# Kernel optimization log

Measured on AMD Instinct MI355X. Metric: run time of the kernel, lower is better.

Reference implementation:

```python
import jax, jax.numpy as jnp
import numpy as np

VOCAB = 16000   # code_size
EMBED = 16
HID = 256
B, T = 64, 128


def _glorot(key, shape, fan):
    return jax.random.normal(key, shape, dtype=jnp.float32) / np.sqrt(fan)


def setup_inputs() -> dict:
    key = jax.random.key(0)
    ks = jax.random.split(key, 20)
    inp = {
        "tokens": jax.random.randint(ks[0], (B, T), 0, VOCAB),
        "h0": jax.random.normal(ks[1], (B, HID), dtype=jnp.float32),
        "c0": jax.random.normal(ks[2], (B, HID), dtype=jnp.float32),
        "emb": jax.random.normal(ks[3], (VOCAB, EMBED), dtype=jnp.float32),
        # LSTMCell params, PyTorch layout: W_ih [4H, in], W_hh [4H, H], biases [4H]
        "Wih1": _glorot(ks[4], (4 * HID, EMBED), EMBED),
        "Whh1": _glorot(ks[5], (4 * HID, HID), HID),
        "bih1": jnp.zeros((4 * HID,), jnp.float32),
        "bhh1": jnp.zeros((4 * HID,), jnp.float32),
        "Wih2": _glorot(ks[6], (4 * HID, HID), HID),
        "Whh2": _glorot(ks[7], (4 * HID, HID), HID),
        "bih2": jnp.zeros((4 * HID,), jnp.float32),
        "bhh2": jnp.zeros((4 * HID,), jnp.float32),
        "Wih3": _glorot(ks[8], (4 * HID, HID), HID),
        "Whh3": _glorot(ks[9], (4 * HID, HID), HID),
        "bih3": jnp.zeros((4 * HID,), jnp.float32),
        "bhh3": jnp.zeros((4 * HID,), jnp.float32),
        # head: Linear(HID,HID) -> ReLU -> Linear(HID,VOCAB)
        "W1": _glorot(ks[10], (HID, HID), HID),
        "b1": jnp.zeros((HID,), jnp.float32),
        "W2": _glorot(ks[11], (VOCAB, HID), HID),
        "b2": jnp.zeros((VOCAB,), jnp.float32),
    }
    return inp


def _lstm_cell(x, h, c, Wih, Whh, bih, bhh):
    # PyTorch LSTMCell gate order: i, f, g, o
    gates = x @ Wih.T + bih + h @ Whh.T + bhh          # [B, 4H]
    i, f, g, o = jnp.split(gates, 4, axis=-1)
    i, f, o = jax.nn.sigmoid(i), jax.nn.sigmoid(f), jax.nn.sigmoid(o)
    g = jnp.tanh(g)
    c_new = f * c + i * g
    h_new = o * jnp.tanh(c_new)
    return h_new, c_new


def reference(tokens, h0, c0, emb,
              Wih1, Whh1, bih1, bhh1,
              Wih2, Whh2, bih2, bhh2,
              Wih3, Whh3, bih3, bhh3,
              W1, b1, W2, b2):
    Bn, Tn = tokens.shape
    x = emb[tokens]                       # [B, T, E]
    xs = jnp.swapaxes(x, 0, 1)            # [T, B, E] for scan over time

    def step(carry, x_t):
        h1, c1, h2, c2, h3, c3 = carry
        h1, c1 = _lstm_cell(x_t, h1, c1, Wih1, Whh1, bih1, bhh1)
        h2, c2 = _lstm_cell(h1, h2, c2, Wih2, Whh2, bih2, bhh2)
        h3, c3 = _lstm_cell(h2, h3, c3, Wih3, Whh3, bih3, bhh3)
        score = jax.nn.relu(h3 @ W1.T + b1) @ W2.T + b2   # [B, V]
        return (h1, c1, h2, c2, h3, c3), score

    init = (h0, c0, h0, c0, h0, c0)       # hidden1 = hidden2 = hidden3 = hidden
    _, scores = jax.lax.scan(step, init, xs)              # [T, B, V]
    scores = jnp.swapaxes(scores, 0, 1).reshape(Bn * Tn, -1)
    labels = tokens.reshape(-1)
    return scores, labels
```

## Files before the change

kernel.cpp:

```cpp
#include <hip/hip_runtime.h>
#include <hip/hip_bf16.h>
#include <stdint.h>

#define T_SEQ 128
#define BATCH 64
#define HIDN  256
#define EMB   16
#define VOCAB 16000
#define HSTR  40

typedef __attribute__((ext_vector_type(8))) short short8v;
typedef __attribute__((ext_vector_type(4))) float f32x4;
typedef __attribute__((ext_vector_type(4))) unsigned short us4v;
typedef unsigned short ushort_t;
typedef unsigned long long u64_t;

#define OFF_WC1    0
#define OFF_WC2    131072
#define OFF_WC3    393216
#define OFF_BS2    655360
#define OFF_BS3    656384
#define OFF_FLAGS  657408
#define OFF_W1T    658432
#define OFF_H3     723968
#define OFF_S1     2821120
#define OFF_W2BF   3869696

#define OUT_XG     0
#define OUT_RINGS  8388608

#define RING_STRIDE 2113536
#define SLOT 16384

__device__ __forceinline__ ushort_t f2bf(float x) {
    __hip_bfloat16 h = __float2bfloat16(x);
    return *reinterpret_cast<ushort_t*>(&h);
}

__device__ __forceinline__ float dpp_x1(float x) {
    return __builtin_bit_cast(float, __builtin_amdgcn_mov_dpp(
        __builtin_bit_cast(int, x), 0xB1, 0xF, 0xF, true));
}
__device__ __forceinline__ float dpp_x2(float x) {
    return __builtin_bit_cast(float, __builtin_amdgcn_mov_dpp(
        __builtin_bit_cast(int, x), 0x4E, 0xF, 0xF, true));
}
__device__ __forceinline__ f32x4 dpp4_x1(f32x4 v) {
    f32x4 r; r[0]=dpp_x1(v[0]); r[1]=dpp_x1(v[1]); r[2]=dpp_x1(v[2]); r[3]=dpp_x1(v[3]); return r;
}
__device__ __forceinline__ f32x4 dpp4_x2(f32x4 v) {
    f32x4 r; r[0]=dpp_x2(v[0]); r[1]=dpp_x2(v[1]); r[2]=dpp_x2(v[2]); r[3]=dpp_x2(v[3]); return r;
}

__device__ __forceinline__ void spin_ge(const int* p, int target) {
    while (__hip_atomic_load(p, __ATOMIC_RELAXED, __HIP_MEMORY_SCOPE_AGENT) < target) {}
}

__device__ __forceinline__ f32x4 bypass_ld128(const void* p) {
    f32x4 v;
    asm volatile("global_load_dwordx4 %0, %1, off sc0 sc1" : "=v"(v) : "v"((uint64_t)p));
    return v;
}
__device__ __forceinline__ void bypass_st128(void* p, f32x4 v) {
    asm volatile("global_store_dwordx4 %0, %1, off sc0 sc1" :: "v"((uint64_t)p), "v"(v) : "memory");
}
__device__ __forceinline__ void vm_drain() {
    asm volatile("s_waitcnt vmcnt(0)" ::: "memory");
    __builtin_amdgcn_sched_barrier(0);
}
__device__ __forceinline__ void lgkm_drain() {
    asm volatile("s_waitcnt lgkmcnt(0)" ::: "memory");
    __builtin_amdgcn_sched_barrier(0);
}

__global__ void k_reset_flags(float* wsf) {
    ((int*)(wsf + OFF_FLAGS))[threadIdx.x] = 0;
}

__global__ void k_reorder_w(const float* __restrict__ Whh1,
                            const float* __restrict__ Wih2, const float* __restrict__ Whh2,
                            const float* __restrict__ Wih3, const float* __restrict__ Whh3,
                            float* __restrict__ wsf) {
    int bid = blockIdx.x;
    int layer = bid >> 10, c = bid & 1023;
    int wgi = c >> 7, rr = c & 127, jl = rr >> 2, gg = rr & 3;
    int row = gg * 256 + wgi * 32 + jl;
    int tid = threadIdx.x;
    if (layer == 0) {
        ushort_t* dst = (ushort_t*)(wsf + OFF_WC1) + (size_t)c * 256;
        dst[tid] = f2bf(Whh1[row * 256 + tid]);
    } else {
        const float* Wi = (layer == 1) ? Wih2 : Wih3;
        const float* Wh = (layer == 1) ? Whh2 : Whh3;
        ushort_t* dst = (ushort_t*)(wsf + ((layer == 1) ? OFF_WC2 : OFF_WC3)) + (size_t)c * 512;
        for (int k = tid; k < 512; k += 256)
            dst[k] = f2bf(k < 256 ? Wi[row * 256 + k] : Wh[row * 256 + k - 256]);
    }
}

__global__ void k_bias23(const float* __restrict__ bi2, const float* __restrict__ bh2,
                         const float* __restrict__ bi3, const float* __restrict__ bh3,
                         float* __restrict__ wsf) {
    int idx = blockIdx.x * 256 + threadIdx.x;
    int layer = idx >> 10, c = idx & 1023;
    int wgi = c >> 7, rr = c & 127, jl = rr >> 2, gg = rr & 3;
    int row = gg * 256 + wgi * 32 + jl;
    wsf[((layer == 0) ? OFF_BS2 : OFF_BS3) + c] =
        (layer == 0) ? (bi2[row] + bh2[row]) : (bi3[row] + bh3[row]);
}

__global__ void k_xg(const int* __restrict__ tokens, const float* __restrict__ emb,
                     const float* __restrict__ Wih1, const float* __restrict__ bih1,
                     const float* __restrict__ bhh1, float* __restrict__ xg) {
    int t = blockIdx.x, cg = blockIdx.y;
    int tid = threadIdx.x;
    __shared__ float xs[64][16];
    for (int idx = tid; idx < 1024; idx += 256) {
        int b = idx >> 4, e = idx & 15;
        xs[b][e] = emb[(size_t)tokens[b * T_SEQ + t] * 16 + e];
    }
    __syncthreads();
    int c = cg * 64 + (tid & 63);
    int b0 = (tid >> 6) * 16;
    int wgi = c >> 7, rr = c & 127, jl = rr >> 2, gg = rr & 3;
    int row = gg * 256 + wgi * 32 + jl;
    float wv[16];
    #pragma unroll
    for (int e = 0; e < 16; ++e) wv[e] = Wih1[row * 16 + e];
    float bias = bih1[row] + bhh1[row];
    float* dst = xg + ((size_t)t * 1024 + c) * 64 + b0;
    for (int b = 0; b < 16; ++b) {
        float s = bias;
        #pragma unroll
        for (int e = 0; e < 16; ++e) s += xs[b0 + b][e] * wv[e];
        dst[b] = s;
    }
}

__global__ void k_init_rings(const float* __restrict__ h0, ushort_t* __restrict__ rbase) {
    int idx = blockIdx.x * 256 + threadIdx.x;
    ushort_t v = f2bf(h0[idx]);
    rbase[idx] = v;
    rbase[RING_STRIDE + idx] = v;
    rbase[2 * RING_STRIDE + idx] = v;
}

__global__ void k_transpose_w1(const float* __restrict__ src, float* __restrict__ dst) {
    int idx = blockIdx.x * 256 + threadIdx.x;
    int n = idx & 255, k = idx >> 8;
    dst[idx] = src[n * 256 + k];
}

__global__ void k_conv_w2(const float* __restrict__ src, ushort_t* __restrict__ dst, int n) {
    int idx = blockIdx.x * 256 + threadIdx.x;
    if (idx < n) dst[idx] = f2bf(src[idx]);
}

template<int LAYER, int NKS>
__device__ __forceinline__ void lstm_body(
    int wg, int tid, const float* __restrict__ c0,
    float* __restrict__ wsf, float* __restrict__ outf,
    ushort_t* hA, ushort_t* hB, ushort_t* hS) {
    const int w = tid >> 6, lane = tid & 63, lr = lane & 15, lg = lane >> 4;
    const int g = lr & 3;
    const int K = NKS * 32;
    const ushort_t* WC = (const ushort_t*)(wsf + (LAYER == 0 ? OFF_WC1 : LAYER == 1 ? OFF_WC2 : OFF_WC3));
    int* fl = (int*)(wsf + OFF_FLAGS);
    ushort_t* H3b = (ushort_t*)(wsf + OFF_H3);
    const float* xg = outf + OUT_XG;
    ushort_t* rbase = (ushort_t*)(outf + OUT_RINGS);
    ushort_t* ringIn = rbase + (size_t)(LAYER == 0 ? 0 : LAYER - 1) * RING_STRIDE;
    ushort_t* ringOwn = rbase + (size_t)LAYER * RING_STRIDE;

    const int ccol = wg * 128 + 2 * w * 16 + lr;
    short8v wr0[NKS], wr1[NKS];
    #pragma unroll
    for (int ks = 0; ks < NKS; ++ks) {
        wr0[ks] = *(const short8v*)(WC + (size_t)ccol * K + ks * 32 + lg * 8);
        wr1[ks] = *(const short8v*)(WC + (size_t)(ccol + 16) * K + ks * 32 + lg * 8);
    }
    float bs0 = 0.f, bs1 = 0.f;
    if (LAYER > 0) {
        const float* BS = wsf + (LAYER == 1 ? OFF_BS2 : OFF_BS3);
        bs0 = BS[ccol]; bs1 = BS[ccol + 16];
    }
    const int jj0 = w * 8 + (lr >> 2);
    const int j0 = wg * 32 + jj0;
    f32x4 cst[4][2];
    #pragma unroll
    for (int i = 0; i < 4; ++i)
        #pragma unroll
        for (int r = 0; r < 4; ++r) {
            cst[i][0][r] = c0[(i * 16 + lg * 4 + r) * 256 + j0];
            cst[i][1][r] = c0[(i * 16 + lg * 4 + r) * 256 + j0 + 4];
        }

    const float sOwn = (g == 2) ? 2.f : -1.f;
    const float aOwn = (g == 2) ? -2.f : 1.f;
    const float bOwn = (g == 2) ? 1.f : 0.f;

    for (int t = 0; t < T_SEQ; ++t) {
        f32x4 xpre[8];
        if (LAYER == 0) {
            const float* xt = xg + ((size_t)t * 1024 + wg * 128) * 64;
            #pragma unroll
            for (int i = 0; i < 4; ++i) {
                xpre[i]     = *(const f32x4*)(xt + (size_t)(2 * w * 16 + lr) * 64 + i * 16 + lg * 4);
                xpre[i + 4] = *(const f32x4*)(xt + (size_t)((2 * w + 1) * 16 + lr) * 64 + i * 16 + lg * 4);
            }
        }
        if (LAYER == 0) {
            if (tid < 8) spin_ge(&fl[tid], t);
        } else {
            if (tid < 16) {
                int idx = tid & 7;
                const int* p = (tid < 8) ? &fl[(LAYER - 1) * 8 + idx] : &fl[LAYER * 8 + idx];
                spin_ge(p, (tid < 8) ? t + 1 : t);
            }
        }
        __syncthreads();
        {
            const char* sA = (const char*)(LAYER == 0 ? (ringOwn + (size_t)t * SLOT)
                                                      : (ringIn + (size_t)(t + 1) * SLOT));
            f32x4 ta[8], tb[8];
            #pragma unroll
            for (int it = 0; it < 8; ++it)
                ta[it] = bypass_ld128(sA + it * 4096 + tid * 16);
            if (LAYER > 0) {
                const char* sB = (const char*)(ringOwn + (size_t)t * SLOT);
                #pragma unroll
                for (int it = 0; it < 8; ++it)
                    tb[it] = bypass_ld128(sB + it * 4096 + tid * 16);
            }
            vm_drain();
            #pragma unroll
            for (int it = 0; it < 8; ++it) {
                int e16 = it * 256 + tid;
                int row = e16 >> 5, c16 = e16 & 31;
                int off = row * 512 + ((c16 ^ (row & 15)) << 4);
                *(f32x4*)((char*)hA + off) = ta[it];
                if (LAYER > 0) *(f32x4*)((char*)hB + off) = tb[it];
            }
        }
        __syncthreads();
        f32x4 acc[4][2];
        if (LAYER == 0) {
            #pragma unroll
            for (int i = 0; i < 4; ++i) { acc[i][0] = xpre[i]; acc[i][1] = xpre[i + 4]; }
        } else {
            #pragma unroll
            for (int i = 0; i < 4; ++i) {
                acc[i][0] = (f32x4){bs0, bs0, bs0, bs0};
                acc[i][1] = (f32x4){bs1, bs1, bs1, bs1};
            }
        }
        #pragma unroll
        for (int i = 0; i < 4; ++i) {
            #pragma unroll
            for (int ks = 0; ks < NKS; ++ks) {
                const ushort_t* hsrc = (ks < 8) ? hA : hB;
                const int krem = ks & 7;
                short8v a = *(const short8v*)((const char*)hsrc + (i * 16 + lr) * 512 +
                                              (((krem * 4 + lg) ^ lr) << 4));
                acc[i][0] = __builtin_amdgcn_mfma_f32_16x16x32_bf16(a, wr0[ks], acc[i][0], 0, 0, 0);
                acc[i][1] = __builtin_amdgcn_mfma_f32_16x16x32_bf16(a, wr1[ks], acc[i][1], 0, 0, 0);
            }
        }
        #pragma unroll
        for (int i = 0; i < 4; ++i) {
            #pragma unroll
            for (int f = 0; f < 2; ++f) {
                f32x4 av = acc[i][f];
                f32x4 act;
                #pragma unroll
                for (int r = 0; r < 4; ++r) {
                    float e = __expf(sOwn * av[r]);
                    act[r] = fmaf(aOwn, __builtin_amdgcn_rcpf(1.f + e), bOwn);
                }
                f32x4 q1 = dpp4_x1(act), q2 = dpp4_x2(act), q3 = dpp4_x1(q2);
                f32x4 gI = (g == 0) ? act : (g == 1) ? q1 : (g == 2) ? q2 : q3;
                f32x4 gF = (g == 1) ? act : (g == 0) ? q1 : (g == 3) ? q2 : q3;
                f32x4 gG = (g == 2) ? act : (g == 3) ? q1 : (g == 0) ? q2 : q3;
                f32x4 gO = (g == 3) ? act : (g == 2) ? q1 : (g == 1) ? q2 : q3;
                f32x4 cv = gF * cst[i][f] + gI * gG;
                cst[i][f] = cv;
                float cg = (g == 0) ? cv[0] : (g == 1) ? cv[1] : (g == 2) ? cv[2] : cv[3];
                float go = (g == 0) ? gO[0] : (g == 1) ? gO[1] : (g == 2) ? gO[2] : gO[3];
                float e2 = __expf(2.f * cg);
                float th = fmaf(-2.f, __builtin_amdgcn_rcpf(1.f + e2), 1.f);
                float hval = go * th;
                int brow = i * 16 + lg * 4 + g;
                hS[brow * HSTR + jj0 + f * 4] = f2bf(hval);
            }
        }
        lgkm_drain();
        {
            f32x4 hv4 = *(const f32x4*)((const char*)hS + lane * (HSTR * 2) + w * 16);
            bypass_st128(ringOwn + (size_t)(t + 1) * SLOT + (size_t)lane * 256 + wg * 32 + w * 8, hv4);
            if (LAYER == 2)
                *(f32x4*)(H3b + (((size_t)lane * 128 + t) * 256 + wg * 32 + w * 8)) = hv4;
        }
        vm_drain();
        __syncthreads();
        if (tid == 0)
            __hip_atomic_store(&fl[LAYER * 8 + wg], t + 1, __ATOMIC_RELAXED, __HIP_MEMORY_SCOPE_AGENT);
    }
}

__global__ __launch_bounds__(256, 1) void k_lstm(const float* __restrict__ c0,
                                                 float* __restrict__ wsf,
                                                 float* __restrict__ outf) {
    __shared__ __align__(16) ushort_t hA[16384];
    __shared__ __align__(16) ushort_t hB[16384];
    __shared__ __align__(16) ushort_t hS[64 * HSTR];
    int layer = blockIdx.x >> 3, wg = blockIdx.x & 7;
    if (layer == 0)      lstm_body<0, 8>(wg, threadIdx.x, c0, wsf, outf, hA, hB, hS);
    else if (layer == 1) lstm_body<1, 16>(wg, threadIdx.x, c0, wsf, outf, hA, hB, hS);
    else                 lstm_body<2, 16>(wg, threadIdx.x, c0, wsf, outf, hA, hB, hS);
}

__global__ __launch_bounds__(256) void k_head1(const ushort_t* __restrict__ H3, const float* __restrict__ W1T,
                                               const float* __restrict__ b1, ushort_t* __restrict__ S1) {
    int tid = threadIdx.x;
    int r0 = blockIdx.x * 32;
    __shared__ float hs[32][256];
    {
        const short8v* src = (const short8v*)(H3 + (size_t)r0 * 256);
        float* hsf = &hs[0][0];
        for (int i = tid; i < 1024; i += 256) {
            short8v v = src[i];
            #pragma unroll
            for (int e = 0; e < 8; ++e) {
                unsigned int u = (unsigned int)(unsigned short)v[e];
                hsf[i * 8 + e] = __uint_as_float(u << 16);
            }
        }
    }
    __syncthreads();
    int c0i = (tid & 63) * 4;
    int rg = (tid >> 6) * 8;
    f32x4 bias = *(const f32x4*)(b1 + c0i);
    f32x4 acc[8];
    #pragma unroll
    for (int r = 0; r < 8; ++r) acc[r] = bias;
    for (int k = 0; k < 256; ++k) {
        f32x4 wv = *(const f32x4*)(W1T + (size_t)k * 256 + c0i);
        #pragma unroll
        for (int r = 0; r < 8; ++r) acc[r] += hs[rg + r][k] * wv;
    }
    #pragma unroll
    for (int r = 0; r < 8; ++r) {
        int row = r0 + rg + r;
        f32x4 v = acc[r];
        us4v u;
        u.x = f2bf(fmaxf(v[0], 0.f));
        u.y = f2bf(fmaxf(v[1], 0.f));
        u.z = f2bf(fmaxf(v[2], 0.f));
        u.w = f2bf(fmaxf(v[3], 0.f));
        *(us4v*)(S1 + (size_t)row * 256 + c0i) = u;
    }
}

__global__ __launch_bounds__(256) void k_head2(const ushort_t* __restrict__ S1,
                                               const ushort_t* __restrict__ W2,
                                               const float* __restrict__ b2, float* __restrict__ out) {
    __shared__ __align__(16) ushort_t As[128][32];
    __shared__ __align__(16) ushort_t Bs[128][32];
    int tid = threadIdx.x;
    int n0 = blockIdx.x * 128;
    int m0 = blockIdx.y * 128;
    int wave = tid >> 6, lane = tid & 63;
    int lr = lane & 15, lg = lane >> 4;
    int wm = (wave >> 1) * 64, wn = (wave & 1) * 64;
    f32x4 acc[4][4] = {};

    for (int kk = 0; kk < 256; kk += 32) {
        int id = tid;
        #pragma unroll
        for (int rep = 0; rep < 2; ++rep, id += 256) {
            int r = id >> 2, ch = (id & 3) * 8;
            *(short8v*)(&As[r][ch]) = *(const short8v*)(S1 + (size_t)(m0 + r) * 256 + kk + ch);
            *(short8v*)(&Bs[r][ch]) = *(const short8v*)(W2 + (size_t)(n0 + r) * 256 + kk + ch);
        }
        __syncthreads();
        short8v a[4], bb[4];
        #pragma unroll
        for (int i = 0; i < 4; ++i) a[i]  = *(const short8v*)(&As[wm + i * 16 + lr][lg * 8]);
        #pragma unroll
        for (int i = 0; i < 4; ++i) bb[i] = *(const short8v*)(&Bs[wn + i * 16 + lr][lg * 8]);
        #pragma unroll
        for (int i = 0; i < 4; ++i)
            #pragma unroll
            for (int f = 0; f < 4; ++f)
                acc[i][f] = __builtin_amdgcn_mfma_f32_16x16x32_bf16(a[i], bb[f], acc[i][f], 0, 0, 0);
        __syncthreads();
    }
    #pragma unroll
    for (int f = 0; f < 4; ++f) {
        int col = n0 + wn + f * 16 + lr;
        float bias = b2[col];
        #pragma unroll
        for (int i = 0; i < 4; ++i) {
            int rowb = m0 + wm + i * 16 + lg * 4;
            #pragma unroll
            for (int r = 0; r < 4; ++r)
                out[(size_t)(rowb + r) * VOCAB + col] = acc[i][f][r] + bias;
        }
    }
}

__global__ void k_labels(const int* __restrict__ tokens, float* __restrict__ out) {
    int i = blockIdx.x * 256 + threadIdx.x;
    if (i < BATCH * T_SEQ) out[i] = (float)tokens[i];
}

extern "C" void kernel_launch(void* const* d_in, const int* in_sizes, int n_in,
                              void* d_out, int out_size, void* d_ws, size_t ws_size,
                              hipStream_t stream) {
    const int*   tokens = (const int*)d_in[0];
    const float* h0   = (const float*)d_in[1];
    const float* c0   = (const float*)d_in[2];
    const float* emb  = (const float*)d_in[3];
    const float* Wih1 = (const float*)d_in[4];
    const float* Whh1 = (const float*)d_in[5];
    const float* bih1 = (const float*)d_in[6];
    const float* bhh1 = (const float*)d_in[7];
    const float* Wih2 = (const float*)d_in[8];
    const float* Whh2 = (const float*)d_in[9];
    const float* bih2 = (const float*)d_in[10];
    const float* bhh2 = (const float*)d_in[11];
    const float* Wih3 = (const float*)d_in[12];
    const float* Whh3 = (const float*)d_in[13];
    const float* bih3 = (const float*)d_in[14];
    const float* bhh3 = (const float*)d_in[15];
    const float* W1   = (const float*)d_in[16];
    const float* b1   = (const float*)d_in[17];
    const float* W2   = (const float*)d_in[18];
    const float* b2   = (const float*)d_in[19];

    float* ws  = (float*)d_ws;
    float* out = (float*)d_out;

    k_reset_flags<<<1, 64, 0, stream>>>(ws);
    k_reorder_w<<<3072, 256, 0, stream>>>(Whh1, Wih2, Whh2, Wih3, Whh3, ws);
    k_bias23<<<8, 256, 0, stream>>>(bih2, bhh2, bih3, bhh3, ws);
    k_xg<<<dim3(128, 16), 256, 0, stream>>>(tokens, emb, Wih1, bih1, bhh1, out + OUT_XG);
    k_init_rings<<<64, 256, 0, stream>>>(h0, (ushort_t*)(out + OUT_RINGS));
    k_transpose_w1<<<256, 256, 0, stream>>>(W1, ws + OFF_W1T);
    k_conv_w2<<<16000, 256, 0, stream>>>(W2, (ushort_t*)(ws + OFF_W2BF), VOCAB * 256);

    k_lstm<<<24, 256, 0, stream>>>(c0, ws, out);

    k_head1<<<256, 256, 0, stream>>>((const ushort_t*)(ws + OFF_H3), ws + OFF_W1T, b1, (ushort_t*)(ws + OFF_S1));
    dim3 g2(125, 64);
    k_head2<<<g2, 256, 0, stream>>>((const ushort_t*)(ws + OFF_S1),
                                    (const ushort_t*)(ws + OFF_W2BF), b2, out);
    k_labels<<<32, 256, 0, stream>>>(tokens, out + (size_t)BATCH * T_SEQ * VOCAB);
}
```

Before: 1.192 ms.

## Replace flag-based inter-block sync with poisoned ring slots polled directly

Removes the per-step atomic flag handshake (spin on flags, store drain, barrier, flag store) between LSTM workgroups. Instead, ring slots are pre-filled with a NaN-like poison pattern by a new kernel, and consumers repeatedly reload the slot until no poisoned value remains, so the data itself acts as the ready signal. This cuts a round trip and a barrier from each timestep's critical path. It adds a large poison-fill kernel and relies on 16-byte stores being observed atomically and on the check of one halfword per vector being enough. It also assumes real bf16 hidden values never equal the poison pattern.

```diff
diff --git a/kernel.cpp b/kernel.cpp
--- a/kernel.cpp
+++ b/kernel.cpp
@@ -8,19 +8,19 @@
 #define EMB   16
 #define VOCAB 16000
 #define HSTR  40
+#define POIS  0x7FC1
 
 typedef __attribute__((ext_vector_type(8))) short short8v;
 typedef __attribute__((ext_vector_type(4))) float f32x4;
+typedef __attribute__((ext_vector_type(4))) int   i32x4;
 typedef __attribute__((ext_vector_type(4))) unsigned short us4v;
 typedef unsigned short ushort_t;
-typedef unsigned long long u64_t;
 
 #define OFF_WC1    0
 #define OFF_WC2    131072
 #define OFF_WC3    393216
 #define OFF_BS2    655360
 #define OFF_BS3    656384
-#define OFF_FLAGS  657408
 #define OFF_W1T    658432
 #define OFF_H3     723968
 #define OFF_S1     2821120
@@ -52,12 +52,8 @@
     f32x4 r; r[0]=dpp_x2(v[0]); r[1]=dpp_x2(v[1]); r[2]=dpp_x2(v[2]); r[3]=dpp_x2(v[3]); return r;
 }
 
-__device__ __forceinline__ void spin_ge(const int* p, int target) {
-    while (__hip_atomic_load(p, __ATOMIC_RELAXED, __HIP_MEMORY_SCOPE_AGENT) < target) {}
-}
-
-__device__ __forceinline__ f32x4 bypass_ld128(const void* p) {
-    f32x4 v;
+__device__ __forceinline__ i32x4 bypass_ld128(const void* p) {
+    i32x4 v;
     asm volatile("global_load_dwordx4 %0, %1, off sc0 sc1" : "=v"(v) : "v"((uint64_t)p));
     return v;
 }
@@ -73,8 +69,13 @@
     __builtin_amdgcn_sched_barrier(0);
 }
 
-__global__ void k_reset_flags(float* wsf) {
-    ((int*)(wsf + OFF_FLAGS))[threadIdx.x] = 0;
+__global__ void k_poison(ushort_t* __restrict__ rbase) {
+    unsigned int u = blockIdx.x * 256 + threadIdx.x;
+    unsigned int l = u >> 20;
+    unsigned int r = u & 1048575;
+    unsigned int s = 1 + (r >> 13);
+    unsigned int off = r & 8191;
+    ((unsigned int*)(rbase + (size_t)l * RING_STRIDE + (size_t)s * SLOT))[off] = 0x7FC17FC1u;
 }
 
 __global__ void k_reorder_w(const float* __restrict__ Whh1,
@@ -165,7 +166,6 @@
     const int g = lr & 3;
     const int K = NKS * 32;
     const ushort_t* WC = (const ushort_t*)(wsf + (LAYER == 0 ? OFF_WC1 : LAYER == 1 ? OFF_WC2 : OFF_WC3));
-    int* fl = (int*)(wsf + OFF_FLAGS);
     ushort_t* H3b = (ushort_t*)(wsf + OFF_H3);
     const float* xg = outf + OUT_XG;
     ushort_t* rbase = (ushort_t*)(outf + OUT_RINGS);
@@ -209,38 +209,42 @@
                 xpre[i + 4] = *(const f32x4*)(xt + (size_t)((2 * w + 1) * 16 + lr) * 64 + i * 16 + lg * 4);
             }
         }
-        if (LAYER == 0) {
-            if (tid < 8) spin_ge(&fl[tid], t);
-        } else {
-            if (tid < 16) {
-                int idx = tid & 7;
-                const int* p = (tid < 8) ? &fl[(LAYER - 1) * 8 + idx] : &fl[LAYER * 8 + idx];
-                spin_ge(p, (tid < 8) ? t + 1 : t);
-            }
-        }
-        __syncthreads();
+        i32x4 ta[8], tb[8];
         {
             const char* sA = (const char*)(LAYER == 0 ? (ringOwn + (size_t)t * SLOT)
                                                       : (ringIn + (size_t)(t + 1) * SLOT));
-            f32x4 ta[8], tb[8];
-            #pragma unroll
-            for (int it = 0; it < 8; ++it)
-                ta[it] = bypass_ld128(sA + it * 4096 + tid * 16);
-            if (LAYER > 0) {
-                const char* sB = (const char*)(ringOwn + (size_t)t * SLOT);
+            const char* sB = (const char*)(ringOwn + (size_t)t * SLOT);
+            bool bad;
+            do {
                 #pragma unroll
                 for (int it = 0; it < 8; ++it)
-                    tb[it] = bypass_ld128(sB + it * 4096 + tid * 16);
-            }
-            vm_drain();
-            #pragma unroll
-            for (int it = 0; it < 8; ++it) {
-                int e16 = it * 256 + tid;
-                int row = e16 >> 5, c16 = e16 & 31;
-                int off = row * 512 + ((c16 ^ (row & 15)) << 4);
-                *(f32x4*)((char*)hA + off) = ta[it];
-                if (LAYER > 0) *(f32x4*)((char*)hB + off) = tb[it];
-            }
+                    ta[it] = bypass_ld128(sA + it * 4096 + tid * 16);
+                if (LAYER > 0) {
+                    #pragma unroll
+                    for (int it = 0; it < 8; ++it)
+                        tb[it] = bypass_ld128(sB + it * 4096 + tid * 16);
+                }
+                vm_drain();
+                int p = 0;
+                #pragma unroll
+                for (int it = 0; it < 8; ++it)
+                    p |= ((ta[it][0] & 0xFFFF) == POIS);
+                if (LAYER > 0) {
+                    #pragma unroll
+                    for (int it = 0; it < 8; ++it)
+                        p |= ((tb[it][0] & 0xFFFF) == POIS);
+                }
+                bad = __any(p);
+            } while (bad);
+        }
+        __syncthreads();
+        #pragma unroll
+        for (int it = 0; it < 8; ++it) {
+            int e16 = it * 256 + tid;
+            int row = e16 >> 5, c16 = e16 & 31;
+            int off = row * 512 + ((c16 ^ (row & 15)) << 4);
+            *(i32x4*)((char*)hA + off) = ta[it];
+            if (LAYER > 0) *(i32x4*)((char*)hB + off) = tb[it];
         }
         __syncthreads();
         f32x4 acc[4][2];
@@ -300,10 +304,6 @@
             if (LAYER == 2)
                 *(f32x4*)(H3b + (((size_t)lane * 128 + t) * 256 + wg * 32 + w * 8)) = hv4;
         }
-        vm_drain();
-        __syncthreads();
-        if (tid == 0)
-            __hip_atomic_store(&fl[LAYER * 8 + wg], t + 1, __ATOMIC_RELAXED, __HIP_MEMORY_SCOPE_AGENT);
     }
 }
 
@@ -441,7 +441,7 @@
     float* ws  = (float*)d_ws;
     float* out = (float*)d_out;
 
-    k_reset_flags<<<1, 64, 0, stream>>>(ws);
+    k_poison<<<12288, 256, 0, stream>>>((ushort_t*)(out + OUT_RINGS));
     k_reorder_w<<<3072, 256, 0, stream>>>(Whh1, Wih2, Whh2, Wih3, Whh3, ws);
     k_bias23<<<8, 256, 0, stream>>>(bih2, bhh2, bih3, bhh3, ws);
     k_xg<<<dim3(128, 16), 256, 0, stream>>>(tokens, emb, Wih1, bih1, bhh1, out + OUT_XG);
```

Result: faster. 1.132 ms (-5.0%).
